# Kernel tuning notes

Measured on AMD Instinct MI355X. Metric: run time of the kernel, lower is better.

## Reference

```python
import jax, jax.numpy as jnp
import numpy as np

FEATURE_DIM = 4
H_PATCHES = 16
W_PATCHES = 16
PATCH_H = 16
PATCH_W = 16
D = FEATURE_DIM * PATCH_H * PATCH_W  # 1024
N = 2 * H_PATCHES * W_PATCHES        # 512
M = 256
B = 64
EPS = 1e-5


def layernorm(x, g, b):
    mu = jnp.mean(x, axis=-1, keepdims=True)
    var = jnp.var(x, axis=-1, keepdims=True)
    return (x - mu) * jax.lax.rsqrt(var + EPS) * g + b


def box3x3(x):
    # per-channel 3x3 window sum with zero padding == diagonal conv in BCIM
    p = jnp.pad(x, ((0, 0), (0, 0), (1, 1), (1, 1)))
    H, W = x.shape[2], x.shape[3]
    return sum(p[:, :, i:i + H, j:j + W] for i in range(3) for j in range(3))


def setup_inputs() -> dict:
    key = jax.random.key(0)
    ks = jax.random.split(key, 20)
    rn = lambda k, shp, s=0.02: (jax.random.normal(k, shp, dtype=jnp.float32) * s)
    inp = {
        'p_vector': jax.random.normal(ks[0], (B, N, D), dtype=jnp.float32),
        'object_vector': jax.random.normal(ks[1], (M, D), dtype=jnp.float32),
        'ln_p_g': 1.0 + rn(ks[2], (D,), 0.1), 'ln_p_b': rn(ks[3], (D,)),
        'ln_o_g': 1.0 + rn(ks[4], (D,), 0.1), 'ln_o_b': rn(ks[5], (D,)),
        'Wq': rn(ks[6], (D, D)), 'bq': rn(ks[7], (D,)),
        'Wk': rn(ks[8], (D, D)), 'bk': rn(ks[9], (D,)),
        'Wv': rn(ks[10], (D, D)), 'bv': rn(ks[11], (D,)),
        'W1': rn(ks[12], (D, D)), 'b1': rn(ks[13], (D,)),
        'ln1_g': 1.0 + rn(ks[14], (D,), 0.1), 'ln1_b': rn(ks[15], (D,)),
        'W2': rn(ks[16], (D, D)), 'b2': rn(ks[17], (D,)),
        'ln2_g': 1.0 + rn(ks[18], (D,), 0.1), 'ln2_b': rn(ks[19], (D,)),
    }
    return inp


def reference(p_vector, object_vector, ln_p_g, ln_p_b, ln_o_g, ln_o_b,
              Wq, bq, Wk, bk, Wv, bv, W1, b1, ln1_g, ln1_b,
              W2, b2, ln2_g, ln2_b):
    # cross-attention (single head, full D)
    p = layernorm(p_vector, ln_p_g, ln_p_b)            # [B,N,D]
    o = layernorm(object_vector, ln_o_g, ln_o_b)       # [M,D]
    q = jnp.einsum('bnd,de->bne', p, Wq) + bq
    k = o @ Wk + bk                                    # [M,D]
    v = o @ Wv + bv
    A = jax.nn.softmax(jnp.einsum('bnd,md->bnm', q, k), axis=-1)
    p = p + jnp.einsum('bnm,md->bnd', A, v)
    # projection block: Linear->LN->GELU->Linear->LN->GELU, residual
    h = jax.nn.gelu(layernorm(jnp.einsum('bnd,de->bne', p, W1) + b1, ln1_g, ln1_b), approximate=False)
    h = jax.nn.gelu(layernorm(jnp.einsum('bnd,de->bne', h, W2) + b2, ln2_g, ln2_b), approximate=False)
    p = p + h
    # BCIM: reshape to image of 2D channels
    x = jnp.transpose(p, (0, 2, 1)).reshape(B, 2 * D, H_PATCHES, W_PATCHES)
    norm = jnp.linalg.norm(x, axis=1, keepdims=True)
    unit = x / norm
    win = box3x3(unit) / 9.0
    sim = jnp.sum(unit * win, axis=1, keepdims=True)   # [B,1,hp,wp]
    x = x * sim
    # reshape back to [B, 2*hp*wp, D]
    x = jnp.transpose(x, (0, 2, 3, 1)).reshape(B, H_PATCHES, W_PATCHES, D, 2)
    x = jnp.transpose(x, (0, 4, 1, 2, 3)).reshape(B, 2 * H_PATCHES * W_PATCHES, D)
    return x
```

## Files before the change

### kernel.cpp

```cpp
#include <hip/hip_runtime.h>
#include <math.h>

#define D_DIM 1024
#define M_DIM 256
#define B_IMG 64
#define N_TOK 512
#define BN    32768

typedef unsigned short u16;
typedef __attribute__((ext_vector_type(8))) __bf16 bf16x8;
typedef __attribute__((ext_vector_type(4))) float  f32x4;

__device__ __forceinline__ u16 f2bf(float f) {
  union { float f; unsigned u; } c; c.f = f;
  unsigned u = c.u;
  return (u16)((u + 0x7FFFu + ((u >> 16) & 1u)) >> 16);
}
__device__ __forceinline__ float bf2f(u16 h) {
  union { unsigned u; float f; } c; c.u = ((unsigned)h) << 16;
  return c.f;
}

__global__ __launch_bounds__(64) void detect_dtype(const u16* __restrict__ p, int* __restrict__ dflag)
{
  const int lane = threadIdx.x;
  const float a = fabsf(bf2f(p[lane * 2]));
  const bool sane = (a >= 1e-20f && a <= 1e3f);
  const unsigned long long m = __ballot(sane);
  if (lane == 0) *dflag = (m == ~0ull) ? 0 : 1;
}

__device__ __forceinline__ float load_in(const void* p, size_t i, int f) {
  return f ? ((const float*)p)[i] : bf2f(((const u16*)p)[i]);
}

template<int EPI>
__global__ __launch_bounds__(256) void gemm_bt(
    const u16* __restrict__ X0, const u16* __restrict__ X1, const u16* __restrict__ X2,
    const u16* __restrict__ Bt0, const u16* __restrict__ Bt1, const u16* __restrict__ Bt2,
    const void* __restrict__ bias, const int* __restrict__ dflag,
    int np_base, int np_extra,
    const u16* res_hi, const u16* res_lo,
    float* outf, u16* outb, u16* outb2,
    int R, int K, int NC)
{
  __shared__ u16 lA[128 * 64];
  __shared__ u16 lB[128 * 64];
  const int tid  = threadIdx.x;
  const int wave = tid >> 6, lane = tid & 63;
  const int quad = lane >> 4, l15 = lane & 15;
  const int wr = wave & 1, wc = wave >> 1;
  const int rblk = blockIdx.x, cblk = blockIdx.y;

  const int np = np_base + (np_extra ? np_extra * (*dflag) : 0);

  const int srow = lane >> 3;
  const int scol = ((lane & 7) ^ (srow & 7)) * 8;

  const u16* Xs[3] = {X0, X1, X2};
  const u16* Bs[3] = {Bt0, Bt1, Bt2};

  f32x4 acc[4][4] = {};

  for (int p = 0; p < np; ++p) {
    const u16* gA = Xs[p] + (size_t)(rblk * 128 + srow) * K + scol;
    const u16* gB = Bs[p] + (size_t)(cblk * 128 + srow) * K + scol;
    for (int k0 = 0; k0 < K; k0 += 64) {
#pragma unroll
      for (int i = 0; i < 4; ++i) {
        const int j = i * 4 + wave;
        __builtin_amdgcn_global_load_lds(
            (const __attribute__((address_space(1))) void*)(gA + (size_t)j * 8 * K + k0),
            (__attribute__((address_space(3))) void*)(lA + j * 512), 16, 0, 0);
        __builtin_amdgcn_global_load_lds(
            (const __attribute__((address_space(1))) void*)(gB + (size_t)j * 8 * K + k0),
            (__attribute__((address_space(3))) void*)(lB + j * 512), 16, 0, 0);
      }
      __syncthreads();
#pragma unroll
      for (int s = 0; s < 2; ++s) {
        bf16x8 af[4], bfr[4];
#pragma unroll
        for (int r = 0; r < 4; ++r) {
          const int row  = wr * 64 + r * 16 + l15;
          const int slot = (s * 4 + quad) ^ (row & 7);
          af[r] = *(const bf16x8*)(lA + row * 64 + slot * 8);
        }
#pragma unroll
        for (int c = 0; c < 4; ++c) {
          const int row  = wc * 64 + c * 16 + l15;
          const int slot = (s * 4 + quad) ^ (row & 7);
          bfr[c] = *(const bf16x8*)(lB + row * 64 + slot * 8);
        }
#pragma unroll
        for (int r = 0; r < 4; ++r)
#pragma unroll
          for (int c = 0; c < 4; ++c)
            acc[r][c] = __builtin_amdgcn_mfma_f32_16x16x32_bf16(af[r], bfr[c], acc[r][c], 0, 0, 0);
      }
      __syncthreads();
    }
  }

  const int fdt = bias ? *dflag : 0;
  const int crow0 = rblk * 128 + wr * 64;
  const int ccol0 = cblk * 128 + wc * 64;
#pragma unroll
  for (int c = 0; c < 4; ++c) {
    const int col = ccol0 + c * 16 + l15;
    const float bcol = bias ? load_in(bias, col, fdt) : 0.0f;
#pragma unroll
    for (int r = 0; r < 4; ++r) {
#pragma unroll
      for (int t = 0; t < 4; ++t) {
        const int row = crow0 + r * 16 + quad * 4 + t;
        const size_t idx = (size_t)row * NC + col;
        float v = acc[r][c][t] + bcol;
        if (EPI == 0) {
          outb[idx] = f2bf(v);
        } else if (EPI == 1) {
          outf[idx] = v;
        } else if (EPI == 2) {
          const float p = bf2f(res_hi[idx]) + bf2f(res_lo[idx]) + v;
          const u16 hi = f2bf(p);
          outb[idx]  = hi;
          outb2[idx] = f2bf(p - bf2f(hi));
        } else if (EPI == 3) {
          outb[(size_t)col * R + row] = f2bf(v);
        } else {
          const u16 hi = f2bf(v);
          outb[idx]  = hi;
          outb2[idx] = f2bf(v - bf2f(hi));
        }
      }
    }
  }
}

__global__ __launch_bounds__(256) void ln_row(
    const void* __restrict__ x, const void* __restrict__ g, const void* __restrict__ b,
    const int* __restrict__ dflag, u16* __restrict__ oh, u16* __restrict__ ol)
{
  const int f = *dflag;
  const int row = blockIdx.x, tid = threadIdx.x;
  const int col = tid * 4;
  const size_t base = (size_t)row * 1024 + col;
  float v0, v1, v2, v3;
  if (f) {
    const float4 xv = *(const float4*)((const float*)x + base);
    v0 = xv.x; v1 = xv.y; v2 = xv.z; v3 = xv.w;
  } else {
    const ushort4 xv = *(const ushort4*)((const u16*)x + base);
    v0 = bf2f(xv.x); v1 = bf2f(xv.y); v2 = bf2f(xv.z); v3 = bf2f(xv.w);
  }
  float s  = v0 + v1 + v2 + v3;
  float sq = v0 * v0 + v1 * v1 + v2 * v2 + v3 * v3;
#pragma unroll
  for (int o = 32; o > 0; o >>= 1) { s += __shfl_xor(s, o); sq += __shfl_xor(sq, o); }
  __shared__ float red[8];
  if ((tid & 63) == 0) { red[tid >> 6] = s; red[4 + (tid >> 6)] = sq; }
  __syncthreads();
  s  = red[0] + red[1] + red[2] + red[3];
  sq = red[4] + red[5] + red[6] + red[7];
  const float mean = s * (1.0f / 1024.0f);
  const float var  = sq * (1.0f / 1024.0f) - mean * mean;
  const float rs   = rsqrtf(var + 1e-5f);
  float y[4];
  y[0] = (v0 - mean) * rs * load_in(g, col + 0, f) + load_in(b, col + 0, f);
  y[1] = (v1 - mean) * rs * load_in(g, col + 1, f) + load_in(b, col + 1, f);
  y[2] = (v2 - mean) * rs * load_in(g, col + 2, f) + load_in(b, col + 2, f);
  y[3] = (v3 - mean) * rs * load_in(g, col + 3, f) + load_in(b, col + 3, f);
  ushort4 hv, lv;
  hv.x = f2bf(y[0]); lv.x = f2bf(y[0] - bf2f(hv.x));
  hv.y = f2bf(y[1]); lv.y = f2bf(y[1] - bf2f(hv.y));
  hv.z = f2bf(y[2]); lv.z = f2bf(y[2] - bf2f(hv.z));
  hv.w = f2bf(y[3]); lv.w = f2bf(y[3] - bf2f(hv.w));
  *(ushort4*)(oh + base) = hv;
  *(ushort4*)(ol + base) = lv;
}

template<int MODE>
__global__ __launch_bounds__(256) void ln_gelu(
    const u16* __restrict__ x, const void* __restrict__ g, const void* __restrict__ b,
    const int* __restrict__ dflag,
    const u16* res_hi, const u16* res_lo,
    u16* ob, u16* oh, u16* ol)
{
  const int f = *dflag;
  const int row = blockIdx.x, tid = threadIdx.x;
  const int col = tid * 4;
  const size_t base = (size_t)row * 1024 + col;
  const ushort4 xv = *(const ushort4*)(x + base);
  const float v0 = bf2f(xv.x), v1 = bf2f(xv.y), v2 = bf2f(xv.z), v3 = bf2f(xv.w);
  float s  = v0 + v1 + v2 + v3;
  float sq = v0 * v0 + v1 * v1 + v2 * v2 + v3 * v3;
#pragma unroll
  for (int o = 32; o > 0; o >>= 1) { s += __shfl_xor(s, o); sq += __shfl_xor(sq, o); }
  __shared__ float red[8];
  if ((tid & 63) == 0) { red[tid >> 6] = s; red[4 + (tid >> 6)] = sq; }
  __syncthreads();
  s  = red[0] + red[1] + red[2] + red[3];
  sq = red[4] + red[5] + red[6] + red[7];
  const float mean = s * (1.0f / 1024.0f);
  const float var  = sq * (1.0f / 1024.0f) - mean * mean;
  const float rs   = rsqrtf(var + 1e-5f);
  float z[4], h[4];
  z[0] = (v0 - mean) * rs * load_in(g, col + 0, f) + load_in(b, col + 0, f);
  z[1] = (v1 - mean) * rs * load_in(g, col + 1, f) + load_in(b, col + 1, f);
  z[2] = (v2 - mean) * rs * load_in(g, col + 2, f) + load_in(b, col + 2, f);
  z[3] = (v3 - mean) * rs * load_in(g, col + 3, f) + load_in(b, col + 3, f);
#pragma unroll
  for (int i = 0; i < 4; ++i)
    h[i] = 0.5f * z[i] * (1.0f + erff(z[i] * 0.70710678118654752f));
  if (MODE == 0) {
    *(ushort4*)(ob + base) = make_ushort4(f2bf(h[0]), f2bf(h[1]), f2bf(h[2]), f2bf(h[3]));
  } else {
    const ushort4 rh = *(const ushort4*)(res_hi + base);
    const ushort4 rl = *(const ushort4*)(res_lo + base);
    float p[4];
    p[0] = bf2f(rh.x) + bf2f(rl.x) + h[0];
    p[1] = bf2f(rh.y) + bf2f(rl.y) + h[1];
    p[2] = bf2f(rh.z) + bf2f(rl.z) + h[2];
    p[3] = bf2f(rh.w) + bf2f(rl.w) + h[3];
    ushort4 hv, lv;
    hv.x = f2bf(p[0]); lv.x = f2bf(p[0] - bf2f(hv.x));
    hv.y = f2bf(p[1]); lv.y = f2bf(p[1] - bf2f(hv.y));
    hv.z = f2bf(p[2]); lv.z = f2bf(p[2] - bf2f(hv.z));
    hv.w = f2bf(p[3]); lv.w = f2bf(p[3] - bf2f(hv.w));
    *(ushort4*)(oh + base) = hv;
    *(ushort4*)(ol + base) = lv;
  }
}

__global__ __launch_bounds__(256) void softmax256(const float* __restrict__ S, u16* __restrict__ A)
{
  const int tid = threadIdx.x, lane = tid & 63, wave = tid >> 6;
  const size_t row = (size_t)blockIdx.x * 4 + wave;
  const float4 v = *(const float4*)(S + row * 256 + lane * 4);
  float m = fmaxf(fmaxf(v.x, v.y), fmaxf(v.z, v.w));
#pragma unroll
  for (int o = 32; o > 0; o >>= 1) m = fmaxf(m, __shfl_xor(m, o));
  const float e0 = expf(v.x - m), e1 = expf(v.y - m), e2 = expf(v.z - m), e3 = expf(v.w - m);
  float s = e0 + e1 + e2 + e3;
#pragma unroll
  for (int o = 32; o > 0; o >>= 1) s += __shfl_xor(s, o);
  const float r = 1.0f / s;
  *(ushort4*)(A + row * 256 + lane * 4) =
      make_ushort4(f2bf(e0 * r), f2bf(e1 * r), f2bf(e2 * r), f2bf(e3 * r));
}

__global__ __launch_bounds__(256) void wtrans5(
    const void* w0, const void* w1, const void* w2, const void* w3, const void* w4,
    u16* h0, u16* h1, u16* h2, u16* h3, u16* h4,
    u16* l0, u16* l1, u16* l2, u16* l3, u16* l4,
    const int* __restrict__ dflag)
{
  const int f = *dflag;
  const void* W; u16* H; u16* L;
  switch (blockIdx.z) {
    case 0: W = w0; H = h0; L = l0; break;
    case 1: W = w1; H = h1; L = l1; break;
    case 2: W = w2; H = h2; L = l2; break;
    case 3: W = w3; H = h3; L = l3; break;
    default: W = w4; H = h4; L = l4; break;
  }
  __shared__ u16 th[32][33];
  __shared__ u16 tl[32][33];
  const int tx = threadIdx.x & 31, ty = threadIdx.x >> 5;
  const int bx = blockIdx.x, by = blockIdx.y;
#pragma unroll
  for (int i = 0; i < 4; ++i) {
    const int r = ty + i * 8;
    const float v = load_in(W, ((size_t)by * 32 + r) * 1024 + bx * 32 + tx, f);
    const u16 hi = f2bf(v);
    th[r][tx] = hi;
    tl[r][tx] = f2bf(v - bf2f(hi));
  }
  __syncthreads();
#pragma unroll
  for (int i = 0; i < 4; ++i) {
    const int r = ty + i * 8;
    const size_t o = ((size_t)bx * 32 + r) * 1024 + by * 32 + tx;
    H[o] = th[tx][r];
    L[o] = tl[tx][r];
  }
}

__global__ __launch_bounds__(256) void zerof(float* p, int n)
{
  const int i = blockIdx.x * 256 + threadIdx.x;
  if (i < n) p[i] = 0.0f;
}

__global__ __launch_bounds__(256) void bcim_dots(
    const u16* __restrict__ p2h, const u16* __restrict__ p2l, float* __restrict__ G)
{
  const int b = blockIdx.x, ds = blockIdx.y;
  __shared__ float T[512][17];
  float acc[9] = {0, 0, 0, 0, 0, 0, 0, 0, 0};
  const int tid = threadIdx.x;
  const int px = tid & 15, py = tid >> 4;
  for (int ch = 0; ch < 8; ++ch) {
    const int d0 = ds * 128 + ch * 16;
#pragma unroll
    for (int i = 0; i < 8; ++i) {
      const int j = i * 256 + tid;
      const int r = j >> 2, q4 = j & 3;
      const size_t base = ((size_t)b * 512 + r) * 1024 + d0 + q4 * 4;
      const ushort4 hv = *(const ushort4*)(p2h + base);
      const ushort4 lv = *(const ushort4*)(p2l + base);
      T[r][q4 * 4 + 0] = bf2f(hv.x) + bf2f(lv.x);
      T[r][q4 * 4 + 1] = bf2f(hv.y) + bf2f(lv.y);
      T[r][q4 * 4 + 2] = bf2f(hv.z) + bf2f(lv.z);
      T[r][q4 * 4 + 3] = bf2f(hv.w) + bf2f(lv.w);
    }
    __syncthreads();
    float a0[16], a1[16];
#pragma unroll
    for (int dc = 0; dc < 16; ++dc) { a0[dc] = T[tid][dc]; a1[dc] = T[tid + 256][dc]; }
#pragma unroll
    for (int o = 0; o < 9; ++o) {
      const int dy = o / 3 - 1, dx = o % 3 - 1;
      const int qx = px + dx, qy = py + dy;
      if (qx >= 0 && qx < 16 && qy >= 0 && qy < 16) {
        const int qp = qy * 16 + qx;
        float sum = 0.0f;
#pragma unroll
        for (int dc = 0; dc < 16; ++dc)
          sum += a0[dc] * T[qp][dc] + a1[dc] * T[qp + 256][dc];
        acc[o] += sum;
      }
    }
    __syncthreads();
  }
#pragma unroll
  for (int o = 0; o < 9; ++o)
    atomicAdd(&G[((size_t)b * 9 + o) * 256 + tid], acc[o]);
}

__global__ __launch_bounds__(256) void bcim_sim_k(const float* __restrict__ G, float* __restrict__ sim)
{
  const int b = blockIdx.x, tid = threadIdx.x;
  __shared__ float nrm[256];
  const float nv = sqrtf(G[((size_t)b * 9 + 4) * 256 + tid]);
  nrm[tid] = nv;
  __syncthreads();
  const int px = tid & 15, py = tid >> 4;
  float s = 0.0f;
#pragma unroll
  for (int o = 0; o < 9; ++o) {
    const int dy = o / 3 - 1, dx = o % 3 - 1;
    const int qx = px + dx, qy = py + dy;
    if (qx >= 0 && qx < 16 && qy >= 0 && qy < 16)
      s += G[((size_t)b * 9 + o) * 256 + tid] / (nv * nrm[qy * 16 + qx]);
  }
  sim[b * 256 + tid] = s * (1.0f / 9.0f);
}

__global__ __launch_bounds__(256) void bcim_scale(
    const u16* __restrict__ p2h, const u16* __restrict__ p2l,
    const float* __restrict__ sim, float* __restrict__ out)
{
  const size_t i4 = (size_t)blockIdx.x * 256 + threadIdx.x;
  const size_t base = i4 * 4;
  const ushort4 hv = *(const ushort4*)(p2h + base);
  const ushort4 lv = *(const ushort4*)(p2l + base);
  const size_t n = base >> 10;
  const size_t b = n >> 9;
  const int pix = (int)(n & 255);
  const float s = sim[b * 256 + pix];
  *(float4*)(out + base) = make_float4(
      (bf2f(hv.x) + bf2f(lv.x)) * s, (bf2f(hv.y) + bf2f(lv.y)) * s,
      (bf2f(hv.z) + bf2f(lv.z)) * s, (bf2f(hv.w) + bf2f(lv.w)) * s);
}

extern "C" void kernel_launch(void* const* d_in, const int* in_sizes, int n_in,
                              void* d_out, int out_size, void* d_ws, size_t ws_size,
                              hipStream_t stream)
{
  (void)in_sizes; (void)n_in; (void)out_size; (void)ws_size;
  const void* p_vector      = d_in[0];
  const void* object_vector = d_in[1];
  const void* ln_p_g = d_in[2];
  const void* ln_p_b = d_in[3];
  const void* ln_o_g = d_in[4];
  const void* ln_o_b = d_in[5];
  const void* Wq = d_in[6];  const void* bq = d_in[7];
  const void* Wk = d_in[8];  const void* bk = d_in[9];
  const void* Wv = d_in[10]; const void* bv = d_in[11];
  const void* W1 = d_in[12]; const void* b1 = d_in[13];
  const void* ln1_g = d_in[14]; const void* ln1_b = d_in[15];
  const void* W2 = d_in[16]; const void* b2 = d_in[17];
  const void* ln2_g = d_in[18]; const void* ln2_b = d_in[19];
  float* out = (float*)d_out;

  char* ws = (char*)d_ws;
  size_t off = 0;
  auto alloc = [&](size_t bytes) -> void* {
    void* p = ws + off;
    off += (bytes + 255) & ~(size_t)255;
    return p;
  };
  int* dflag = (int*)alloc(256);
  u16* WqH = (u16*)alloc((size_t)D_DIM * D_DIM * 2);
  u16* WkH = (u16*)alloc((size_t)D_DIM * D_DIM * 2);
  u16* WvH = (u16*)alloc((size_t)D_DIM * D_DIM * 2);
  u16* W1H = (u16*)alloc((size_t)D_DIM * D_DIM * 2);
  u16* W2H = (u16*)alloc((size_t)D_DIM * D_DIM * 2);
  u16* WqL = (u16*)alloc((size_t)D_DIM * D_DIM * 2);
  u16* WkL = (u16*)alloc((size_t)D_DIM * D_DIM * 2);
  u16* WvL = (u16*)alloc((size_t)D_DIM * D_DIM * 2);
  u16* W1L = (u16*)alloc((size_t)D_DIM * D_DIM * 2);
  u16* W2L = (u16*)alloc((size_t)D_DIM * D_DIM * 2);
  u16* PH = (u16*)alloc((size_t)BN * D_DIM * 2);
  u16* PL = (u16*)alloc((size_t)BN * D_DIM * 2);
  u16* QH = (u16*)alloc((size_t)BN * D_DIM * 2);
  u16* QL = (u16*)alloc((size_t)BN * D_DIM * 2);
  float* S_f = (float*)alloc((size_t)BN * M_DIM * 4);
  u16* A_b   = (u16*)alloc((size_t)BN * M_DIM * 2);
  u16* onH = (u16*)alloc((size_t)M_DIM * D_DIM * 2);
  u16* onL = (u16*)alloc((size_t)M_DIM * D_DIM * 2);
  u16* kH  = (u16*)alloc((size_t)M_DIM * D_DIM * 2);
  u16* kL  = (u16*)alloc((size_t)M_DIM * D_DIM * 2);
  u16* vT  = (u16*)alloc((size_t)D_DIM * M_DIM * 2);
  float* G   = (float*)alloc((size_t)B_IMG * 9 * 256 * 4);
  float* sim = (float*)alloc((size_t)B_IMG * 256 * 4);

  detect_dtype<<<1, 64, 0, stream>>>((const u16*)p_vector, dflag);
  wtrans5<<<dim3(32, 32, 5), 256, 0, stream>>>(Wq, Wk, Wv, W1, W2,
      WqH, WkH, WvH, W1H, W2H, WqL, WkL, WvL, W1L, W2L, dflag);
  zerof<<<(B_IMG * 9 * 256 + 255) / 256, 256, 0, stream>>>(G, B_IMG * 9 * 256);

  ln_row<<<BN, 256, 0, stream>>>(p_vector, ln_p_g, ln_p_b, dflag, PH, PL);
  ln_row<<<M_DIM, 256, 0, stream>>>(object_vector, ln_o_g, ln_o_b, dflag, onH, onL);

  gemm_bt<4><<<dim3(2, 8), 256, 0, stream>>>(onH, onL, onH, WkH, WkH, WkL,
      bk, dflag, 2, 1, nullptr, nullptr, nullptr, kH, kL, M_DIM, D_DIM, D_DIM);
  gemm_bt<3><<<dim3(2, 8), 256, 0, stream>>>(onH, onL, onH, WvH, WvH, WvL,
      bv, dflag, 2, 1, nullptr, nullptr, nullptr, vT, nullptr, M_DIM, D_DIM, D_DIM);
  gemm_bt<4><<<dim3(256, 8), 256, 0, stream>>>(PH, PL, PH, WqH, WqH, WqL,
      bq, dflag, 2, 1, nullptr, nullptr, nullptr, QH, QL, BN, D_DIM, D_DIM);

  gemm_bt<1><<<dim3(256, 2), 256, 0, stream>>>(QH, QL, QH, kH, kH, kL,
      nullptr, dflag, 3, 0, nullptr, nullptr, S_f, nullptr, nullptr, BN, D_DIM, M_DIM);
  softmax256<<<BN / 4, 256, 0, stream>>>(S_f, A_b);

  gemm_bt<2><<<dim3(256, 8), 256, 0, stream>>>(A_b, nullptr, nullptr, vT, nullptr, nullptr,
      nullptr, dflag, 1, 0, PH, PL, nullptr, PH, PL, BN, M_DIM, D_DIM);

  gemm_bt<0><<<dim3(256, 8), 256, 0, stream>>>(PH, nullptr, nullptr, W1H, nullptr, nullptr,
      b1, dflag, 1, 0, nullptr, nullptr, nullptr, QH, nullptr, BN, D_DIM, D_DIM);
  ln_gelu<0><<<BN, 256, 0, stream>>>(QH, ln1_g, ln1_b, dflag, nullptr, nullptr, QL, nullptr, nullptr);

  gemm_bt<0><<<dim3(256, 8), 256, 0, stream>>>(QL, nullptr, nullptr, W2H, nullptr, nullptr,
      b2, dflag, 1, 0, nullptr, nullptr, nullptr, QH, nullptr, BN, D_DIM, D_DIM);
  ln_gelu<1><<<BN, 256, 0, stream>>>(QH, ln2_g, ln2_b, dflag, PH, PL, nullptr, PH, PL);

  bcim_dots<<<dim3(B_IMG, 8), 256, 0, stream>>>(PH, PL, G);
  bcim_sim_k<<<B_IMG, 256, 0, stream>>>(G, sim);
  bcim_scale<<<(BN * D_DIM / 4) / 256, 256, 0, stream>>>(PH, PL, sim, out);
}
```

Before: 1.503 ms.

## Add 256x256-tile double-buffered GEMM with direct global-to-LDS loads for the large matmuls

```diff
diff --git a/kernel.cpp b/kernel.cpp
--- a/kernel.cpp
+++ b/kernel.cpp
@@ -127,6 +127,127 @@
           outb2[idx] = f2bf(p - bf2f(hi));
         } else if (EPI == 3) {
           outb[(size_t)col * R + row] = f2bf(v);
+        } else {
+          const u16 hi = f2bf(v);
+          outb[idx]  = hi;
+          outb2[idx] = f2bf(v - bf2f(hi));
+        }
+      }
+    }
+  }
+}
+
+template<int EPI>
+__global__ __launch_bounds__(512, 2) void gemm256(
+    const u16* __restrict__ X0, const u16* __restrict__ X1, const u16* __restrict__ X2,
+    const u16* __restrict__ Bt0, const u16* __restrict__ Bt1, const u16* __restrict__ Bt2,
+    const void* __restrict__ bias, const int* __restrict__ dflag,
+    int np_base, int np_extra,
+    const u16* res_hi, const u16* res_lo,
+    float* outf, u16* outb, u16* outb2,
+    int R, int K, int NC)
+{
+  extern __shared__ u16 lds2[];
+  const int tid  = threadIdx.x;
+  const int wave = tid >> 6, lane = tid & 63;
+  const int quad = lane >> 4, l15 = lane & 15;
+  const int wm = wave >> 2, wn = wave & 3;
+  const int rblk = blockIdx.x, cblk = blockIdx.y;
+
+  const int np = np_base + (np_extra ? np_extra * (*dflag) : 0);
+  const int ktiles = K >> 6;
+  const int ktl = 31 - __builtin_clz(ktiles);
+  const int NT = np << ktl;
+
+  const u16* Xs[3] = {X0, X1, X2};
+  const u16* Bs[3] = {Bt0, Bt1, Bt2};
+
+  const int srow = lane >> 3;
+  const int scol = ((lane & 7) ^ srow) * 8;
+
+  f32x4 acc[8][4] = {};
+
+  auto stage = [&](int t) {
+    const int p  = t >> ktl;
+    const int k0 = (t & (ktiles - 1)) << 6;
+    const u16* gA = Xs[p] + (size_t)(rblk * 256 + srow) * K + k0 + scol;
+    const u16* gB = Bs[p] + (size_t)(cblk * 256 + srow) * K + k0 + scol;
+    u16* dst = lds2 + (t & 1) * 32768;
+#pragma unroll
+    for (int i = 0; i < 4; ++i) {
+      const int r0 = i * 64 + wave * 8;
+      __builtin_amdgcn_global_load_lds(
+          (const __attribute__((address_space(1))) void*)(gA + (size_t)r0 * K),
+          (__attribute__((address_space(3))) void*)(dst + r0 * 64), 16, 0, 0);
+      __builtin_amdgcn_global_load_lds(
+          (const __attribute__((address_space(1))) void*)(gB + (size_t)r0 * K),
+          (__attribute__((address_space(3))) void*)(dst + 16384 + r0 * 64), 16, 0, 0);
+    }
+  };
+
+  stage(0);
+  stage(1);
+  asm volatile("s_waitcnt vmcnt(8)" ::: "memory");
+  asm volatile("s_barrier" ::: "memory");
+
+  for (int t = 0; t < NT; ++t) {
+    const u16* bufA = lds2 + (t & 1) * 32768;
+    const u16* bufB = bufA + 16384;
+    __builtin_amdgcn_s_setprio(1);
+#pragma unroll
+    for (int kk = 0; kk < 2; ++kk) {
+      bf16x8 bfr[4];
+#pragma unroll
+      for (int n = 0; n < 4; ++n) {
+        const int row  = wn * 64 + n * 16 + l15;
+        const int slot = (kk * 4 + quad) ^ (row & 7);
+        bfr[n] = *(const bf16x8*)(bufB + row * 64 + slot * 8);
+      }
+#pragma unroll
+      for (int m = 0; m < 8; ++m) {
+        const int row  = wm * 128 + m * 16 + l15;
+        const int slot = (kk * 4 + quad) ^ (row & 7);
+        const bf16x8 a = *(const bf16x8*)(bufA + row * 64 + slot * 8);
+#pragma unroll
+        for (int n = 0; n < 4; ++n)
+          acc[m][n] = __builtin_amdgcn_mfma_f32_16x16x32_bf16(a, bfr[n], acc[m][n], 0, 0, 0);
+      }
+    }
+    __builtin_amdgcn_s_setprio(0);
+    asm volatile("s_barrier" ::: "memory");
+    if (t + 2 < NT) {
+      stage(t + 2);
+      asm volatile("s_waitcnt vmcnt(8)" ::: "memory");
+      asm volatile("s_barrier" ::: "memory");
+    } else if (t + 1 < NT) {
+      asm volatile("s_waitcnt vmcnt(0)" ::: "memory");
+      asm volatile("s_barrier" ::: "memory");
+    }
+  }
+
+  const int fdt = bias ? *dflag : 0;
+  const int crow0 = rblk * 256 + wm * 128;
+  const int ccol0 = cblk * 256 + wn * 64;
+#pragma unroll
+  for (int n = 0; n < 4; ++n) {
+    const int col = ccol0 + n * 16 + l15;
+    const float bcol = bias ? load_in(bias, col, fdt) : 0.0f;
+#pragma unroll
+    for (int m = 0; m < 8; ++m) {
+#pragma unroll
+      for (int u = 0; u < 4; ++u) {
+        const int row = crow0 + m * 16 + quad * 4 + u;
+        const size_t idx = (size_t)row * NC + col;
+        float v = acc[m][n][u] + bcol;
+        if (EPI == 0) {
+          outb[idx] = f2bf(v);
+        } else if (EPI == 1) {
+          outf[idx] = v;
+        } else if (EPI == 2) {
+          const float pp = bf2f(res_hi[idx]) + bf2f(res_lo[idx]) + v;
+          const u16 hi = f2bf(pp);
+          outb[idx]  = hi;
+          outb2[idx] = f2bf(pp - bf2f(hi));
         } else {
           const u16 hi = f2bf(v);
           outb[idx]  = hi;
@@ -438,21 +559,21 @@
       bk, dflag, 2, 1, nullptr, nullptr, nullptr, kH, kL, M_DIM, D_DIM, D_DIM);
   gemm_bt<3><<<dim3(2, 8), 256, 0, stream>>>(onH, onL, onH, WvH, WvH, WvL,
       bv, dflag, 2, 1, nullptr, nullptr, nullptr, vT, nullptr, M_DIM, D_DIM, D_DIM);
-  gemm_bt<4><<<dim3(256, 8), 256, 0, stream>>>(PH, PL, PH, WqH, WqH, WqL,
+  gemm256<4><<<dim3(128, 4), 512, 131072, stream>>>(PH, PL, PH, WqH, WqH, WqL,
       bq, dflag, 2, 1, nullptr, nullptr, nullptr, QH, QL, BN, D_DIM, D_DIM);
 
-  gemm_bt<1><<<dim3(256, 2), 256, 0, stream>>>(QH, QL, QH, kH, kH, kL,
+  gemm256<1><<<dim3(128, 1), 512, 131072, stream>>>(QH, QL, QH, kH, kH, kL,
       nullptr, dflag, 3, 0, nullptr, nullptr, S_f, nullptr, nullptr, BN, D_DIM, M_DIM);
   softmax256<<<BN / 4, 256, 0, stream>>>(S_f, A_b);
 
-  gemm_bt<2><<<dim3(256, 8), 256, 0, stream>>>(A_b, nullptr, nullptr, vT, nullptr, nullptr,
+  gemm256<2><<<dim3(128, 4), 512, 131072, stream>>>(A_b, nullptr, nullptr, vT, nullptr, nullptr,
       nullptr, dflag, 1, 0, PH, PL, nullptr, PH, PL, BN, M_DIM, D_DIM);
 
-  gemm_bt<0><<<dim3(256, 8), 256, 0, stream>>>(PH, nullptr, nullptr, W1H, nullptr, nullptr,
+  gemm256<0><<<dim3(128, 4), 512, 131072, stream>>>(PH, nullptr, nullptr, W1H, nullptr, nullptr,
       b1, dflag, 1, 0, nullptr, nullptr, nullptr, QH, nullptr, BN, D_DIM, D_DIM);
   ln_gelu<0><<<BN, 256, 0, stream>>>(QH, ln1_g, ln1_b, dflag, nullptr, nullptr, QL, nullptr, nullptr);
 
-  gemm_bt<0><<<dim3(256, 8), 256, 0, stream>>>(QL, nullptr, nullptr, W2H, nullptr, nullptr,
+  gemm256<0><<<dim3(128, 4), 512, 131072, stream>>>(QL, nullptr, nullptr, W2H, nullptr, nullptr,
       b2, dflag, 1, 0, nullptr, nullptr, nullptr, QH, nullptr, BN, D_DIM, D_DIM);
   ln_gelu<1><<<BN, 256, 0, stream>>>(QH, ln2_g, ln2_b, dflag, PH, PL, nullptr, PH, PL);
 
```

Measured after the change: 1.566 ms. 1.04x slower.
